# Performance work log

Hardware: AMD Instinct MI355X
Metric: run time of the kernel (lower is better)

## Reference

```python
import jax, jax.numpy as jnp
import numpy as np

K_GRAD = 20        # num_nbrs for gradient operator
K_NORMAL = 10      # knn for normal/basis estimation
GRAD_REG = 1e-3    # grad_reg (lambda)
KERNEL_WIDTH = 1.0 # grad_kernel_width
EPS = 1e-8
N1, N2 = 8192, 8192
CHANNELS = [3, 64, 128, 256]


def knn_idx(pos, k):
    # brute-force kNN incl. self (loop=True, target_to_source)
    sq = jnp.sum(pos * pos, axis=1)
    d2 = sq[:, None] + sq[None, :] - 2.0 * (pos @ pos.T)
    _, idx = jax.lax.top_k(-d2, k)
    return idx  # [N, k]


def estimate_basis(pos, nbr, orientation):
    rel = pos[nbr] - pos[:, None, :]              # [N,k,3]
    cov = jnp.einsum('nki,nkj->nij', rel, rel)    # [N,3,3] local PCA
    _, vecs = jnp.linalg.eigh(cov)                # ascending eigenvalues
    normal, x_basis = vecs[:, :, 0], vecs[:, :, 2]
    sign = jnp.where(jnp.sum(normal * orientation, -1, keepdims=True) < 0.0, -1.0, 1.0)
    normal = normal * sign                        # orient along `orientation`
    y_basis = jnp.cross(normal, x_basis)
    return normal, x_basis, y_basis


def build_grad_div(pos, x_basis, y_basis, nbr):
    # regularized, Gaussian-weighted least-squares fit of a linear function per neighborhood
    rel = pos[nbr] - pos[:, None, :]              # [N,k,3]
    u = jnp.einsum('nkd,nd->nk', rel, x_basis)    # tangent coords
    v = jnp.einsum('nkd,nd->nk', rel, y_basis)
    dist = jnp.sqrt(jnp.sum(rel * rel, -1) + EPS)
    h = jnp.mean(dist, axis=1, keepdims=True)     # per-point bandwidth
    w = jnp.exp(-(dist * dist) / ((KERNEL_WIDTH * h) ** 2 + EPS))
    B = jnp.stack([jnp.ones_like(u), u, v], -1)   # [N,k,3] design matrix
    BtW = jnp.swapaxes(B, 1, 2) * w[:, None, :]   # [N,3,k]
    A = BtW @ B + GRAD_REG * jnp.eye(3, dtype=pos.dtype)
    C = jnp.linalg.solve(A, BtW)                  # [N,3,k] LS coefficients
    Gx, Gy = C[:, 1, :], C[:, 2, :]               # gradient stencils
    basis = jnp.stack([x_basis, y_basis], -1)     # [N,3,2]
    R = jnp.einsum('nda,nkdb->nkab', basis, basis[nbr])  # transport j->i, [N,k,2,2]
    return Gx, Gy, R


def grad_apply(Gx, Gy, nbr, f):
    fn = f[nbr]                                   # [N,k,C]
    return jnp.stack([jnp.einsum('nk,nkc->nc', Gx, fn),
                      jnp.einsum('nk,nkc->nc', Gy, fn)], 1)  # [N,2,C]


def div_apply(Gx, Gy, R, nbr, v):
    vt = jnp.einsum('nkab,nkbc->nkac', R, v[nbr])  # transported neighbor vectors
    return (jnp.einsum('nk,nkc->nc', Gx, vt[:, :, 0]) +
            jnp.einsum('nk,nkc->nc', Gy, vt[:, :, 1]))


def delta_conv(x, v, nbr, Gx, Gy, R, Ws, bs, Wv, bv, centralized):
    xn = x[nbr]
    if centralized:
        xn = xn - x[:, None, :]
    xmax = jnp.max(xn, axis=1)                    # max aggregation
    dv = div_apply(Gx, Gy, R, nbr, v)             # divergence
    Jv = jnp.stack([-v[:, 1], v[:, 0]], 1)        # 90-degree rotation
    cv = div_apply(Gx, Gy, R, nbr, Jv)            # curl = div(J v)
    x_out = jax.nn.relu(jnp.concatenate([xmax, dv, cv], -1) @ Ws + bs)
    if Wv is None:
        return x_out, v                            # last layer: scalar only
    gv = grad_apply(Gx, Gy, nbr, x_out)           # [N,2,Cout]
    vo = jnp.concatenate([v, gv], -1) @ Wv        # channel mix, no bias (equivariant)
    n = jnp.sqrt(jnp.sum(vo * vo, axis=1, keepdims=True) + EPS)
    vo = vo * (jax.nn.relu(n + bv) / (n + EPS))   # norm-gated vector nonlinearity
    return x_out, vo


def _forward(points, als_ppoints, params):
    pos = jnp.concatenate([points, als_ppoints], axis=0)  # [N,3]
    nbr = knn_idx(pos, K_GRAD)
    nbr_n = knn_idx(pos, K_NORMAL)
    _, xb, yb = estimate_basis(pos, nbr_n, orientation=pos)
    Gx, Gy, R = build_grad_div(pos, xb, yb, nbr)
    x = pos
    v = grad_apply(Gx, Gy, nbr, x)                # v = grad @ x
    out = []
    for i, (Ws, bs, Wv, bv) in enumerate(params):
        x, v = delta_conv(x, v, nbr, Gx, Gy, R, Ws, bs, Wv, bv, centralized=(i == 0))
        out.append(x)
    return tuple(out)


def setup_inputs():
    key = jax.random.key(0)
    ks = jax.random.split(key, 8)
    inp = {
        'points': jax.random.normal(ks[0], (N1, 3), jnp.float32),
        'als_ppoints': jax.random.normal(ks[1], (N2, 3), jnp.float32),
    }
    ki = 2
    for i in range(3):
        cin, cout = CHANNELS[i], CHANNELS[i + 1]
        inp[f'Ws{i}'] = jax.random.normal(ks[ki], (3 * cin, cout), jnp.float32) / np.sqrt(3.0 * cin)
        inp[f'bs{i}'] = jnp.zeros((cout,), jnp.float32)
        ki += 1
        if i < 2:
            inp[f'Wv{i}'] = jax.random.normal(ks[ki], (cin + cout, cout), jnp.float32) / np.sqrt(float(cin + cout))
            inp[f'bv{i}'] = jnp.zeros((cout,), jnp.float32)
            ki += 1
    return inp


def reference(points, als_ppoints, Ws0, bs0, Wv0, bv0, Ws1, bs1, Wv1, bv1, Ws2, bs2):
    params = [(Ws0, bs0, Wv0, bv0), (Ws1, bs1, Wv1, bv1), (Ws2, bs2, None, None)]
    return _forward(points, als_ppoints, params)
```

## Files before the change

### kernel.cpp

```cpp
#include <hip/hip_runtime.h>
#include <math.h>

#define NPTS 16384
#define KG 20
#define KN 10
#define KC 6
#define EPSF 1e-8f

#define GDIM 32
#define GL 4.75f
#define CW 0.296875f
#define GINV 3.3684210526f
#define RMAX 6

typedef __attribute__((ext_vector_type(8))) short short8v;
typedef __attribute__((ext_vector_type(4))) float floatx4;

__device__ __forceinline__ unsigned short f2bf(float v) {
  union { float f; unsigned u; } x;
  x.f = v;
  unsigned r = x.u + 0x7FFFu + ((x.u >> 16) & 1u);
  return (unsigned short)(r >> 16);
}

__device__ __forceinline__ float bf2f(unsigned short u) {
  union { unsigned u32; float f; } x;
  x.u32 = (unsigned)u << 16;
  return x.f;
}

#define KNN_INSERT(d2v, iv)                                                 \
  if ((d2v) < dist[KG - 1]) {                                               \
    dist[KG - 1] = (d2v); idx[KG - 1] = (iv);                               \
    _Pragma("unroll")                                                       \
    for (int s_ = KG - 1; s_ > 0; --s_) {                                   \
      if (dist[s_] < dist[s_ - 1]) {                                        \
        float td_ = dist[s_]; dist[s_] = dist[s_ - 1]; dist[s_ - 1] = td_;  \
        int ti_ = idx[s_]; idx[s_] = idx[s_ - 1]; idx[s_ - 1] = ti_;        \
      }                                                                     \
    }                                                                       \
  }

#define KNN_INSERTC(d2v, iv)                                                \
  if ((d2v) < dist[KC - 1]) {                                               \
    dist[KC - 1] = (d2v); idx[KC - 1] = (iv);                               \
    _Pragma("unroll")                                                       \
    for (int s_ = KC - 1; s_ > 0; --s_) {                                   \
      if (dist[s_] < dist[s_ - 1]) {                                        \
        float td_ = dist[s_]; dist[s_] = dist[s_ - 1]; dist[s_ - 1] = td_;  \
        int ti_ = idx[s_]; idx[s_] = idx[s_ - 1]; idx[s_ - 1] = ti_;        \
      }                                                                     \
    }                                                                       \
  }

__global__ __launch_bounds__(256) void posbin_kernel(const float* __restrict__ pts,
                                                     const float* __restrict__ als,
                                                     float4* __restrict__ pos4,
                                                     int* __restrict__ cell_count,
                                                     int* __restrict__ pt_cell) {
  int n = blockIdx.x * 256 + threadIdx.x;
  if (n >= NPTS) return;
  const float* src = (n < 8192) ? (pts + (size_t)n * 3) : (als + (size_t)(n - 8192) * 3);
  float x = src[0], y = src[1], z = src[2];
  pos4[n] = make_float4(x, y, z, 0.f);
  int cxi = (int)floorf((x + GL) * GINV); cxi = min(max(cxi, 0), GDIM - 1);
  int cyi = (int)floorf((y + GL) * GINV); cyi = min(max(cyi, 0), GDIM - 1);
  int czi = (int)floorf((z + GL) * GINV); czi = min(max(czi, 0), GDIM - 1);
  int c = (czi * GDIM + cyi) * GDIM + cxi;
  pt_cell[n] = c;
  atomicAdd(&cell_count[c], 1);
}

__global__ __launch_bounds__(256) void zero_kernel(int* __restrict__ cell_count,
                                                   int* __restrict__ fb_count) {
  int i = blockIdx.x * 256 + threadIdx.x;
  if (i < GDIM * GDIM * GDIM) cell_count[i] = 0;
  if (i == 0) *fb_count = 0;
}

__device__ __forceinline__ int cell_of(float x) {
  int c = (int)floorf((x + GL) * GINV);
  return min(max(c, 0), GDIM - 1);
}

__global__ __launch_bounds__(1024) void scan_kernel(const int* __restrict__ cell_count,
                                                    int* __restrict__ cell_start,
                                                    int* __restrict__ cell_cursor) {
  __shared__ int s[1024];
  int tid = threadIdx.x;
  int base = tid * 32;
  int local[32];
  int sum = 0;
#pragma unroll
  for (int i = 0; i < 32; ++i) { local[i] = cell_count[base + i]; sum += local[i]; }
  s[tid] = sum;
  __syncthreads();
  for (int off = 1; off < 1024; off <<= 1) {
    int v = (tid >= off) ? s[tid - off] : 0;
    __syncthreads();
    s[tid] += v;
    __syncthreads();
  }
  int run = s[tid] - sum;
#pragma unroll
  for (int i = 0; i < 32; ++i) {
    cell_start[base + i] = run;
    cell_cursor[base + i] = run;
    run += local[i];
  }
}

__global__ __launch_bounds__(256) void scatter_kernel(const float4* __restrict__ pos4,
                                                      const int* __restrict__ pt_cell,
                                                      int* __restrict__ cell_cursor,
                                                      float4* __restrict__ sorted4,
                                                      int* __restrict__ sortmap) {
  int i = blockIdx.x * 256 + threadIdx.x;
  if (i >= NPTS) return;
  int c = pt_cell[i];
  int dst = atomicAdd(&cell_cursor[c], 1);
  float4 p = pos4[i];
  p.w = __int_as_float(i);
  sorted4[dst] = p;
  sortmap[dst] = i;
}

__global__ __launch_bounds__(256) void knn_grid_kernel(const float4* __restrict__ sorted4,
                                                       const int* __restrict__ cell_start,
                                                       const int* __restrict__ cell_count,
                                                       int* __restrict__ nbr,
                                                       int* __restrict__ fb_list,
                                                       int* __restrict__ fb_count) {
  int lane = threadIdx.x & 63;
  int sub = lane >> 5;
  int sl = lane & 31;
  int qs = blockIdx.x * 8 + (threadIdx.x >> 6) * 2 + sub;
  if (qs >= NPTS) return;
  float4 p = sorted4[qs];
  int cx = cell_of(p.x), cy = cell_of(p.y), cz = cell_of(p.z);
  float dist[KC];
  int idx[KC];
#pragma unroll
  for (int i = 0; i < KC; ++i) { dist[i] = 3.4e38f; idx[i] = 0; }

  {
    int tot = 0;
    int x0 = max(cx - 1, 0), x1 = min(cx + 1, GDIM - 1);
    int zlo = max(cz - 1, 0), zhi = min(cz + 1, GDIM - 1);
    int ylo = max(cy - 1, 0), yhi = min(cy + 1, GDIM - 1);
    for (int z = zlo; z <= zhi; ++z) {
      for (int y = ylo; y <= yhi; ++y) {
        int c0 = (z * GDIM + y) * GDIM + x0;
        int c1 = (z * GDIM + y) * GDIM + x1;
        int beg = cell_start[c0];
        int end = cell_start[c1] + cell_count[c1];
        int off = (sl - tot) & 31;
        for (int j = beg + off; j < end; j += 32) {
          float4 sp = sorted4[j];
          float dx = sp.x - p.x, dy = sp.y - p.y, dz = sp.z - p.z;
          float d2 = dx * dx + dy * dy + dz * dz;
          KNN_INSERTC(d2, j);
        }
        tot += end - beg;
      }
    }
  }
  int done;
  {
    float b2 = CW * CW;
    int cnt = 0;
#pragma unroll
    for (int i = 0; i < KC; ++i) cnt += (dist[i] <= b2) ? 1 : 0;
#pragma unroll
    for (int s = 1; s < 32; s <<= 1) cnt += __shfl_xor(cnt, s, 64);
    done = (cnt >= KG) ? 1 : 0;
  }

  for (int r = 2; r <= RMAX && !done; ++r) {
    int side = 2 * r + 1;
    int nt = side * side;
    float rcp = 1.0f / (float)side;
    for (int t = sl; t < nt; t += 32) {
      int qz = (int)(((float)t + 0.5f) * rcp);
      int dz = qz - r;
      int dy = t - qz * side - r;
      int z = cz + dz, y = cy + dy;
      if (z < 0 || z >= GDIM || y < 0 || y >= GDIM) continue;
      int rowbase = (z * GDIM + y) * GDIM;
      if (dz == -r || dz == r || dy == -r || dy == r) {
        int xa = max(cx - r, 0), xb = min(cx + r, GDIM - 1);
        int beg = cell_start[rowbase + xa];
        int end = cell_start[rowbase + xb] + cell_count[rowbase + xb];
        for (int j = beg; j < end; ++j) {
          float4 sp = sorted4[j];
          float ddx = sp.x - p.x, ddy = sp.y - p.y, ddz = sp.z - p.z;
          float d2 = ddx * ddx + ddy * ddy + ddz * ddz;
          KNN_INSERTC(d2, j);
        }
      } else {
        int x = cx - r;
        if (x >= 0) {
          int c = rowbase + x;
          int beg = cell_start[c], end = beg + cell_count[c];
          for (int j = beg; j < end; ++j) {
            float4 sp = sorted4[j];
            float ddx = sp.x - p.x, ddy = sp.y - p.y, ddz = sp.z - p.z;
            float d2 = ddx * ddx + ddy * ddy + ddz * ddz;
            KNN_INSERTC(d2, j);
          }
        }
        x = cx + r;
        if (x < GDIM) {
          int c = rowbase + x;
          int beg = cell_start[c], end = beg + cell_count[c];
          for (int j = beg; j < end; ++j) {
            float4 sp = sorted4[j];
            float ddx = sp.x - p.x, ddy = sp.y - p.y, ddz = sp.z - p.z;
            float d2 = ddx * ddx + ddy * ddy + ddz * ddz;
            KNN_INSERTC(d2, j);
          }
        }
      }
    }
    float b = CW * (float)r;
    float b2 = b * b;
    int cnt = 0;
#pragma unroll
    for (int i = 0; i < KC; ++i) cnt += (dist[i] <= b2) ? 1 : 0;
#pragma unroll
    for (int s = 1; s < 32; s <<= 1) cnt += __shfl_xor(cnt, s, 64);
    if (cnt >= KG) done = 1;
  }

  int popc = 0, ovf = 0;
  for (int round = 0; round < KG; ++round) {
    unsigned long long key = ((unsigned long long)__float_as_uint(dist[0]) << 14) |
                             (unsigned long long)(unsigned)idx[0];
    unsigned long long m = key;
#pragma unroll
    for (int s = 1; s < 32; s <<= 1) {
      unsigned long long o = __shfl_xor(m, s, 64);
      if (o < m) m = o;
    }
    if (key == m) {
      nbr[(size_t)qs * KG + round] = (int)(m & 0x3FFF);
#pragma unroll
      for (int s = 0; s < KC - 1; ++s) { dist[s] = dist[s + 1]; idx[s] = idx[s + 1]; }
      dist[KC - 1] = 3.4e38f;
      idx[KC - 1] = 0;
      if (++popc == KC) ovf = 1;
    }
  }
#pragma unroll
  for (int s = 1; s < 32; s <<= 1) ovf |= __shfl_xor(ovf, s, 64);
  if ((ovf || !done) && sl == 0) {
    int s = atomicAdd(fb_count, 1);
    fb_list[s] = qs;
  }
}

__global__ __launch_bounds__(256) void knn_fb_kernel(const float4* __restrict__ sorted4,
                                                     const int* __restrict__ fb_list,
                                                     const int* __restrict__ fb_count,
                                                     int* __restrict__ nbr) {
  __shared__ unsigned long long lists[256 * KG];
  __shared__ unsigned long long heads[256];
  __shared__ unsigned long long winner;
  int tid = threadIdx.x;
  int cnt = *fb_count;
  for (int qi = blockIdx.x; qi < cnt; qi += gridDim.x) {
    int t = fb_list[qi];
    float4 p = sorted4[t];
    float dist[KG];
    int idx[KG];
#pragma unroll
    for (int i = 0; i < KG; ++i) { dist[i] = 3.4e38f; idx[i] = 0; }
    int j0 = tid * 64;
    for (int j = j0; j < j0 + 64; ++j) {
      float4 c = sorted4[j];
      float dx = c.x - p.x, dy = c.y - p.y, dz = c.z - p.z;
      float d2 = dx * dx + dy * dy + dz * dz;
      KNN_INSERT(d2, j);
    }
#pragma unroll
    for (int i = 0; i < KG; ++i)
      lists[tid * KG + i] = ((unsigned long long)__float_as_uint(dist[i]) << 22) |
                            ((unsigned long long)(unsigned)idx[i] << 8) |
                            (unsigned long long)tid;
    int hp = 0;
    __syncthreads();
    for (int round = 0; round < KG; ++round) {
      heads[tid] = (hp < KG) ? lists[tid * KG + hp] : ~0ull;
      __syncthreads();
      if (tid < 64) {
        unsigned long long m = heads[tid];
        unsigned long long o = heads[tid + 64];  if (o < m) m = o;
        o = heads[tid + 128]; if (o < m) m = o;
        o = heads[tid + 192]; if (o < m) m = o;
#pragma unroll
        for (int s = 32; s > 0; s >>= 1) {
          unsigned long long x = __shfl_xor(m, s, 64);
          if (x < m) m = x;
        }
        if (tid == 0) winner = m;
      }
      __syncthreads();
      unsigned long long w = winner;
      if (tid == (int)(w & 0xFF)) hp++;
      if (tid == 0) nbr[(size_t)t * KG + round] = (int)((w >> 8) & 0x3FFF);
      __syncthreads();
    }
  }
}

__global__ __launch_bounds__(256) void basis_kernel(const float4* __restrict__ sorted4,
                                                    const int* __restrict__ nbr,
                                                    float4* __restrict__ xb4,
                                                    float4* __restrict__ yb4) {
  int n = blockIdx.x * 256 + threadIdx.x;
  if (n >= NPTS) return;
  float4 p = sorted4[n];
  float c00 = 0, c01 = 0, c02 = 0, c11 = 0, c12 = 0, c22 = 0;
  for (int k = 0; k < KN; ++k) {
    int m = nbr[(size_t)n * KG + k];
    float4 pm = sorted4[m];
    float dx = pm.x - p.x, dy = pm.y - p.y, dz = pm.z - p.z;
    c00 += dx * dx; c01 += dx * dy; c02 += dx * dz;
    c11 += dy * dy; c12 += dy * dz; c22 += dz * dz;
  }
  float nx = 0.f, ny = 0.f, nz = 1.f;
  float p1 = c01 * c01 + c02 * c02 + c12 * c12;
  float qm = (c00 + c11 + c22) * (1.f / 3.f);
  float g0 = c00 - qm, g1 = c11 - qm, g2 = c22 - qm;
  float p2 = g0 * g0 + g1 * g1 + g2 * g2 + 2.f * p1;
  if (p2 > 1e-16f) {
    float pp = sqrtf(p2 * (1.f / 6.f));
    float inv = 1.f / pp;
    float b00 = g0 * inv, b11 = g1 * inv, b22 = g2 * inv;
    float b01 = c01 * inv, b02 = c02 * inv, b12 = c12 * inv;
    float detB = b00 * (b11 * b22 - b12 * b12) - b01 * (b01 * b22 - b12 * b02) +
                 b02 * (b01 * b12 - b11 * b02);
    float r = 0.5f * detB;
    r = fminf(1.f, fmaxf(-1.f, r));
    float phi = acosf(r) * (1.f / 3.f);
    float e1 = qm + 2.f * pp * __cosf(phi);
    float e3 = qm + 2.f * pp * __cosf(phi + 2.0943951023931953f);
    float e2 = 3.f * qm - e1 - e3;
    float a00 = c00 - e1, a11 = c11 - e1, a22 = c22 - e1;
    float f00 = c00 - e2, f11 = c11 - e2, f22 = c22 - e2;
    float u0 = a00 * f00 + c01 * c01 + c02 * c02;
    float u1 = c01 * f00 + a11 * c01 + c12 * c02;
    float u2 = c02 * f00 + c12 * c01 + a22 * c02;
    float v0 = a00 * c01 + c01 * f11 + c02 * c12;
    float v1 = c01 * c01 + a11 * f11 + c12 * c12;
    float v2 = c02 * c01 + c12 * f11 + a22 * c12;
    float w0 = a00 * c02 + c01 * c12 + c02 * f22;
    float w1 = c01 * c02 + a11 * c12 + c12 * f22;
    float w2 = c02 * c02 + c12 * c12 + a22 * f22;
    float nu = u0 * u0 + u1 * u1 + u2 * u2;
    float nv = v0 * v0 + v1 * v1 + v2 * v2;
    float nw = w0 * w0 + w1 * w1 + w2 * w2;
    float bx = u0, by = u1, bz = u2, bn = nu;
    if (nv > bn) { bx = v0; by = v1; bz = v2; bn = nv; }
    if (nw > bn) { bx = w0; by = w1; bz = w2; bn = nw; }
    if (bn > 1e-30f) {
      float s = 1.f / sqrtf(bn);
      nx = bx * s; ny = by * s; nz = bz * s;
    }
  }
  float dotp = nx * p.x + ny * p.y + nz * p.z;
  if (dotp < 0.f) { nx = -nx; ny = -ny; nz = -nz; }
  float ax = fabsf(nx), ay = fabsf(ny), az = fabsf(nz);
  float ex = 0.f, ey = 0.f, ez = 0.f;
  if (ax <= ay && ax <= az) ex = 1.f;
  else if (ay <= az) ey = 1.f;
  else ez = 1.f;
  float tx = ny * ez - nz * ey, ty = nz * ex - nx * ez, tz = nx * ey - ny * ex;
  float tn = 1.f / sqrtf(tx * tx + ty * ty + tz * tz);
  tx *= tn; ty *= tn; tz *= tn;
  float ux = ny * tz - nz * ty, uy = nz * tx - nx * tz, uz = nx * ty - ny * tx;
  xb4[n] = make_float4(tx, ty, tz, 0.f);
  yb4[n] = make_float4(ux, uy, uz, 0.f);
}

__global__ __launch_bounds__(256) void graddiv_kernel(const float4* __restrict__ sorted4,
                                                      const int* __restrict__ nbr,
                                                      const float4* __restrict__ xb4,
                                                      const float4* __restrict__ yb4,
                                                      float* __restrict__ Gx,
                                                      float* __restrict__ Gy,
                                                      float2* __restrict__ C2,
                                                      float* __restrict__ v0) {
  int n = blockIdx.x * 256 + threadIdx.x;
  if (n >= NPTS) return;
  float4 p = sorted4[n], xb = xb4[n], yb = yb4[n];
  float u[KG], vv[KG], w[KG];
  int mm[KG];
  float hsum = 0.f;
#pragma unroll
  for (int k = 0; k < KG; ++k) {
    int m = nbr[(size_t)n * KG + k];
    mm[k] = m;
    float4 pm = sorted4[m];
    float rx = pm.x - p.x, ry = pm.y - p.y, rz = pm.z - p.z;
    u[k] = rx * xb.x + ry * xb.y + rz * xb.z;
    vv[k] = rx * yb.x + ry * yb.y + rz * yb.z;
    float dd = sqrtf(rx * rx + ry * ry + rz * rz + EPSF);
    w[k] = dd; hsum += dd;
  }
  float h = hsum * (1.f / KG);
  float invden = 1.f / (h * h + EPSF);
  float A00 = 0, A01 = 0, A02 = 0, A11 = 0, A12 = 0, A22 = 0;
#pragma unroll
  for (int k = 0; k < KG; ++k) {
    float wk = __expf(-(w[k] * w[k]) * invden);
    w[k] = wk;
    A00 += wk; A01 += wk * u[k]; A02 += wk * vv[k];
    A11 += wk * u[k] * u[k]; A12 += wk * u[k] * vv[k];
    A22 += wk * vv[k] * vv[k];
  }
  A00 += 0.001f; A11 += 0.001f; A22 += 0.001f;
  float det = A00 * (A11 * A22 - A12 * A12) - A01 * (A01 * A22 - A12 * A02) +
              A02 * (A01 * A12 - A11 * A02);
  float idet = 1.f / det;
  float i10 = (A02 * A12 - A01 * A22) * idet;
  float i11 = (A00 * A22 - A02 * A02) * idet;
  float i12 = (A01 * A02 - A00 * A12) * idet;
  float i20 = (A01 * A12 - A02 * A11) * idet;
  float i21 = i12;
  float i22 = (A00 * A11 - A01 * A01) * idet;
  float a0x = 0, a0y = 0, a0z = 0, a1x = 0, a1y = 0, a1z = 0;
#pragma unroll
  for (int k = 0; k < KG; ++k) {
    float gx = w[k] * (i10 + i11 * u[k] + i12 * vv[k]);
    float gy = w[k] * (i20 + i21 * u[k] + i22 * vv[k]);
    Gx[(size_t)n * KG + k] = gx;
    Gy[(size_t)n * KG + k] = gy;
    int m = mm[k];
    float4 pm = sorted4[m];
    a0x += gx * pm.x; a0y += gx * pm.y; a0z += gx * pm.z;
    a1x += gy * pm.x; a1y += gy * pm.y; a1z += gy * pm.z;
    float4 xm = xb4[m], ym = yb4[m];
    float g3x = gx * xb.x + gy * yb.x;
    float g3y = gx * xb.y + gy * yb.y;
    float g3z = gx * xb.z + gy * yb.z;
    float ca = g3x * xm.x + g3y * xm.y + g3z * xm.z;
    float cb = g3x * ym.x + g3y * ym.y + g3z * ym.z;
    C2[(size_t)n * KG + k] = make_float2(ca, cb);
  }
  v0[((size_t)n * 2 + 0) * 3 + 0] = a0x;
  v0[((size_t)n * 2 + 0) * 3 + 1] = a0y;
  v0[((size_t)n * 2 + 0) * 3 + 2] = a0z;
  v0[((size_t)n * 2 + 1) * 3 + 0] = a1x;
  v0[((size_t)n * 2 + 1) * 3 + 1] = a1y;
  v0[((size_t)n * 2 + 1) * 3 + 2] = a1z;
}

template <int CENTRAL>
__global__ __launch_bounds__(256) void feat16_kernel(const float* __restrict__ x, int ldx,
                                                     int cin,
                                                     const float* __restrict__ v,
                                                     const int* __restrict__ nbr,
                                                     const float2* __restrict__ C2,
                                                     unsigned short* __restrict__ feat, int Kp) {
  int per = Kp - 2 * cin;
  int gid = blockIdx.x * 256 + threadIdx.x;
  if (gid >= NPTS * per) return;
  int n = gid / per;
  int c = gid - n * per;
  size_t fb = (size_t)n * Kp;
  if (c >= cin) {
    feat[fb + 3 * cin + (c - cin)] = 0;
    return;
  }
  float xc = x[(size_t)n * ldx + c];
  float xmax = -3.4e38f, dv = 0.f, cv = 0.f;
  for (int k = 0; k < KG; ++k) {
    int m = nbr[(size_t)n * KG + k];
    float2 cc = C2[(size_t)n * KG + k];
    float xm = x[(size_t)m * ldx + c];
    xmax = fmaxf(xmax, CENTRAL ? (xm - xc) : xm);
    float va = v[((size_t)m * 2 + 0) * cin + c];
    float vb = v[((size_t)m * 2 + 1) * cin + c];
    dv += cc.x * va + cc.y * vb;
    cv += cc.y * va - cc.x * vb;
  }
  feat[fb + c] = f2bf(xmax);
  feat[fb + cin + c] = f2bf(dv);
  feat[fb + 2 * cin + c] = f2bf(cv);
}

__global__ __launch_bounds__(256) void feat16v8_kernel(const unsigned short* __restrict__ x,
                                                       int cin,
                                                       const unsigned short* __restrict__ v,
                                                       const int* __restrict__ nbr,
                                                       const float2* __restrict__ C2,
                                                       unsigned short* __restrict__ feat) {
  int per = cin >> 3;
  int gid = blockIdx.x * 256 + threadIdx.x;
  if (gid >= NPTS * per) return;
  int n = gid / per;
  int c8 = (gid - n * per) << 3;
  float xmax[8], dv[8], cv[8];
#pragma unroll
  for (int i = 0; i < 8; ++i) { xmax[i] = -3.4e38f; dv[i] = 0.f; cv[i] = 0.f; }
  const int* nrow = nbr + (size_t)n * KG;
  const float2* crow = C2 + (size_t)n * KG;
#pragma unroll 4
  for (int k = 0; k < KG; ++k) {
    int m = nrow[k];
    float2 cc = crow[k];
    short8v xm = *reinterpret_cast<const short8v*>(x + (size_t)m * cin + c8);
    short8v va = *reinterpret_cast<const short8v*>(v + ((size_t)m * 2 + 0) * cin + c8);
    short8v vb = *reinterpret_cast<const short8v*>(v + ((size_t)m * 2 + 1) * cin + c8);
#pragma unroll
    for (int i = 0; i < 8; ++i) {
      float xf = bf2f((unsigned short)xm[i]);
      float af = bf2f((unsigned short)va[i]);
      float bf = bf2f((unsigned short)vb[i]);
      xmax[i] = fmaxf(xmax[i], xf);
      dv[i] += cc.x * af + cc.y * bf;
      cv[i] += cc.y * af - cc.x * bf;
    }
  }
  size_t fb = (size_t)n * (3 * cin);
  short8v o0, o1, o2;
#pragma unroll
  for (int i = 0; i < 8; ++i) {
    o0[i] = (short)f2bf(xmax[i]);
    o1[i] = (short)f2bf(dv[i]);
    o2[i] = (short)f2bf(cv[i]);
  }
  *reinterpret_cast<short8v*>(&feat[fb + c8]) = o0;
  *reinterpret_cast<short8v*>(&feat[fb + cin + c8]) = o1;
  *reinterpret_cast<short8v*>(&feat[fb + 2 * cin + c8]) = o2;
}

__global__ __launch_bounds__(256) void vin16_kernel(const float* __restrict__ v, int cin,
                                                    const unsigned short* __restrict__ xout,
                                                    int cout,
                                                    const int* __restrict__ nbr,
                                                    const float* __restrict__ Gx,
                                                    const float* __restrict__ Gy,
                                                    unsigned short* __restrict__ vinb, int Kp,
                                                    int total) {
  int gid = blockIdx.x * 256 + threadIdx.x;
  if (gid >= total) return;
  int n = gid / Kp;
  int c = gid - n * Kp;
  int K = cin + cout;
  unsigned short o0, o1;
  if (c < cin) {
    o0 = f2bf(v[((size_t)n * 2 + 0) * cin + c]);
    o1 = f2bf(v[((size_t)n * 2 + 1) * cin + c]);
  } else if (c < K) {
    int cc = c - cin;
    float a0 = 0.f, a1 = 0.f;
    for (int k = 0; k < KG; ++k) {
      int m = nbr[(size_t)n * KG + k];
      float f = bf2f(xout[(size_t)m * cout + cc]);
      a0 += Gx[(size_t)n * KG + k] * f;
      a1 += Gy[(size_t)n * KG + k] * f;
    }
    o0 = f2bf(a0);
    o1 = f2bf(a1);
  } else {
    o0 = 0; o1 = 0;
  }
  vinb[((size_t)n * 2 + 0) * Kp + c] = o0;
  vinb[((size_t)n * 2 + 1) * Kp + c] = o1;
}

__global__ __launch_bounds__(256) void vin16v8_kernel(const unsigned short* __restrict__ v,
                                                      int cin,
                                                      const unsigned short* __restrict__ xout,
                                                      int cout,
                                                      const int* __restrict__ nbr,
                                                      const float* __restrict__ Gx,
                                                      const float* __restrict__ Gy,
                                                      unsigned short* __restrict__ vinb,
                                                      int Kp) {
  int per = Kp >> 3;
  int gid = blockIdx.x * 256 + threadIdx.x;
  if (gid >= NPTS * per) return;
  int n = gid / per;
  int c8 = (gid - n * per) << 3;
  short8v o0, o1;
  if (c8 < cin) {
    o0 = *reinterpret_cast<const short8v*>(v + ((size_t)n * 2 + 0) * cin + c8);
    o1 = *reinterpret_cast<const short8v*>(v + ((size_t)n * 2 + 1) * cin + c8);
  } else {
    int cc8 = c8 - cin;
    float a0[8], a1[8];
#pragma unroll
    for (int i = 0; i < 8; ++i) { a0[i] = 0.f; a1[i] = 0.f; }
    const int* nrow = nbr + (size_t)n * KG;
    const float* gxr = Gx + (size_t)n * KG;
    const float* gyr = Gy + (size_t)n * KG;
#pragma unroll 4
    for (int k = 0; k < KG; ++k) {
      int m = nrow[k];
      float gx = gxr[k], gy = gyr[k];
      short8v f = *reinterpret_cast<const short8v*>(xout + (size_t)m * cout + cc8);
#pragma unroll
      for (int i = 0; i < 8; ++i) {
        float ff = bf2f((unsigned short)f[i]);
        a0[i] += gx * ff;
        a1[i] += gy * ff;
      }
    }
#pragma unroll
    for (int i = 0; i < 8; ++i) {
      o0[i] = (short)f2bf(a0[i]);
      o1[i] = (short)f2bf(a1[i]);
    }
  }
  *reinterpret_cast<short8v*>(&vinb[((size_t)n * 2 + 0) * Kp + c8]) = o0;
  *reinterpret_cast<short8v*>(&vinb[((size_t)n * 2 + 1) * Kp + c8]) = o1;
}

__device__ __forceinline__ void wprep_one(const float* W, unsigned short* Wt, int K, int Kp,
                                          int N, int i) {
  int n = i / Kp, k = i - n * Kp;
  Wt[i] = (k < K) ? f2bf(W[(size_t)k * N + n]) : (unsigned short)0;
}

__global__ __launch_bounds__(256) void wprep_all_kernel(const float* __restrict__ Ws0,
                                                        const float* __restrict__ Wv0,
                                                        const float* __restrict__ Ws1,
                                                        const float* __restrict__ Wv1,
                                                        const float* __restrict__ Ws2,
                                                        unsigned short* __restrict__ Wt_s0,
                                                        unsigned short* __restrict__ Wt_v0,
                                                        unsigned short* __restrict__ Wt_s1,
                                                        unsigned short* __restrict__ Wt_v1,
                                                        unsigned short* __restrict__ Wt_s2) {
  int gid = blockIdx.x * 256 + threadIdx.x;
  if (gid < 2048) wprep_one(Ws0, Wt_s0, 9, 32, 64, gid);
  else if (gid < 8192) wprep_one(Wv0, Wt_v0, 67, 96, 64, gid - 2048);
  else if (gid < 32768) wprep_one(Ws1, Wt_s1, 192, 192, 128, gid - 8192);
  else if (gid < 57344) wprep_one(Wv1, Wt_v1, 192, 192, 128, gid - 32768);
  else if (gid < 155648) wprep_one(Ws2, Wt_s2, 384, 384, 256, gid - 57344);
}

template <int MODE>
__global__ __launch_bounds__(256) void gemm16_kernel(const unsigned short* __restrict__ A,
                                                     const unsigned short* __restrict__ Bt,
                                                     const float* __restrict__ bias,
                                                     float* __restrict__ Cf,
                                                     unsigned short* __restrict__ Cb,
                                                     const int* __restrict__ rowmap,
                                                     int Kp, int Ncol) {
  int lane = threadIdx.x & 63;
  int wave = threadIdx.x >> 6;
  int rowBase = blockIdx.y * 64 + wave * 16;
  int colBase = blockIdx.x * 64;
  int lr = lane & 15;
  int kg = (lane >> 4) * 8;
  floatx4 acc0 = {0.f, 0.f, 0.f, 0.f};
  floatx4 acc1 = acc0, acc2 = acc0, acc3 = acc0;
  const unsigned short* arow = A + (size_t)(rowBase + lr) * Kp + kg;
  const unsigned short* b0p = Bt + (size_t)(colBase + lr) * Kp + kg;
  for (int k0 = 0; k0 < Kp; k0 += 32) {
    short8v a = *reinterpret_cast<const short8v*>(arow + k0);
    short8v b0 = *reinterpret_cast<const short8v*>(b0p + k0);
    short8v b1 = *reinterpret_cast<const short8v*>(b0p + (size_t)16 * Kp + k0);
    short8v b2 = *reinterpret_cast<const short8v*>(b0p + (size_t)32 * Kp + k0);
    short8v b3 = *reinterpret_cast<const short8v*>(b0p + (size_t)48 * Kp + k0);
    acc0 = __builtin_amdgcn_mfma_f32_16x16x32_bf16(a, b0, acc0, 0, 0, 0);
    acc1 = __builtin_amdgcn_mfma_f32_16x16x32_bf16(a, b1, acc1, 0, 0, 0);
    acc2 = __builtin_amdgcn_mfma_f32_16x16x32_bf16(a, b2, acc2, 0, 0, 0);
    acc3 = __builtin_amdgcn_mfma_f32_16x16x32_bf16(a, b3, acc3, 0, 0, 0);
  }
  int rsub = (lane >> 4) * 4;
  floatx4 accs[4] = {acc0, acc1, acc2, acc3};
  int orow[4];
  if (MODE == 0) {
#pragma unroll
    for (int r = 0; r < 4; ++r) orow[r] = rowmap[rowBase + rsub + r];
  }
#pragma unroll
  for (int nb = 0; nb < 4; ++nb) {
    int col = colBase + nb * 16 + lr;
    float bb = bias[col];
    if (MODE == 0) {
#pragma unroll
      for (int r = 0; r < 4; ++r) {
        int row = rowBase + rsub + r;
        float val = fmaxf(accs[nb][r] + bb, 0.f);
        Cf[(size_t)orow[r] * Ncol + col] = val;
        if (Cb) Cb[(size_t)row * Ncol + col] = f2bf(val);
      }
    } else {
#pragma unroll
      for (int pr = 0; pr < 2; ++pr) {
        float a0 = accs[nb][2 * pr], a1 = accs[nb][2 * pr + 1];
        float nrm = sqrtf(a0 * a0 + a1 * a1 + EPSF);
        float s = fmaxf(nrm + bb, 0.f) / (nrm + EPSF);
        int row = rowBase + rsub + 2 * pr;
        Cb[(size_t)row * Ncol + col] = f2bf(a0 * s);
        Cb[(size_t)(row + 1) * Ncol + col] = f2bf(a1 * s);
      }
    }
  }
}

extern "C" void kernel_launch(void* const* d_in, const int* in_sizes, int n_in,
                              void* d_out, int out_size, void* d_ws, size_t ws_size,
                              hipStream_t stream) {
  const float* pts = (const float*)d_in[0];
  const float* als = (const float*)d_in[1];
  const float* Ws0 = (const float*)d_in[2];
  const float* bs0 = (const float*)d_in[3];
  const float* Wv0 = (const float*)d_in[4];
  const float* bv0 = (const float*)d_in[5];
  const float* Ws1 = (const float*)d_in[6];
  const float* bs1 = (const float*)d_in[7];
  const float* Wv1 = (const float*)d_in[8];
  const float* bv1 = (const float*)d_in[9];
  const float* Ws2 = (const float*)d_in[10];
  const float* bs2 = (const float*)d_in[11];

  char* ws = (char*)d_ws;
  float4* pos4 = (float4*)(ws + 0);
  int* nbr = (int*)(ws + 262144);
  float4* xb4 = (float4*)(ws + 1572864);
  float4* yb4 = (float4*)(ws + 1835008);
  float* Gx = (float*)(ws + 2097152);
  float* Gy = (float*)(ws + 3407872);
  float2* C2 = (float2*)(ws + 4718592);
  float* v0f = (float*)(ws + 7340032);
  unsigned short* vb_a = (unsigned short*)(ws + 8388608);
  unsigned short* vb_b = (unsigned short*)(ws + 17825792);
  unsigned short* xb0m = (unsigned short*)(ws + 23068672);
  unsigned short* xb1m = (unsigned short*)(ws + 26214400);
  unsigned short* stg = (unsigned short*)(ws + 31457280);
  char* wtb = ws + 45088768;
  unsigned short* Wt_s0 = (unsigned short*)(wtb + 0);
  unsigned short* Wt_v0 = (unsigned short*)(wtb + 4096);
  unsigned short* Wt_s1 = (unsigned short*)(wtb + 16384);
  unsigned short* Wt_v1 = (unsigned short*)(wtb + 65536);
  unsigned short* Wt_s2 = (unsigned short*)(wtb + 114688);

  char* gws = ws + 46137344;
  int* cell_count = (int*)(gws + 0);
  int* cell_start = (int*)(gws + 131072);
  int* cell_cursor = (int*)(gws + 262144);
  int* pt_cell = (int*)(gws + 393216);
  int* fb_list = (int*)(gws + 458752);
  int* fb_count = (int*)(gws + 524288);
  float4* sorted4 = (float4*)(gws + 528384);
  int* sortmap = (int*)(gws + 790528);

  float* out0 = (float*)d_out;
  float* out1 = out0 + (size_t)NPTS * 64;
  float* out2 = out1 + (size_t)NPTS * 128;

  zero_kernel<<<(GDIM * GDIM * GDIM + 255) / 256, 256, 0, stream>>>(cell_count, fb_count);
  posbin_kernel<<<64, 256, 0, stream>>>(pts, als, pos4, cell_count, pt_cell);
  scan_kernel<<<1, 1024, 0, stream>>>(cell_count, cell_start, cell_cursor);
  scatter_kernel<<<64, 256, 0, stream>>>(pos4, pt_cell, cell_cursor, sorted4, sortmap);
  knn_grid_kernel<<<NPTS / 8, 256, 0, stream>>>(sorted4, cell_start, cell_count, nbr, fb_list,
                                                fb_count);
  knn_fb_kernel<<<128, 256, 0, stream>>>(sorted4, fb_list, fb_count, nbr);

  basis_kernel<<<64, 256, 0, stream>>>(sorted4, nbr, xb4, yb4);
  graddiv_kernel<<<64, 256, 0, stream>>>(sorted4, nbr, xb4, yb4, Gx, Gy, C2, v0f);

  wprep_all_kernel<<<608, 256, 0, stream>>>(Ws0, Wv0, Ws1, Wv1, Ws2, Wt_s0, Wt_v0, Wt_s1,
                                            Wt_v1, Wt_s2);

  feat16_kernel<1><<<(NPTS * 26 + 255) / 256, 256, 0, stream>>>((const float*)sorted4, 4, 3,
                                                                v0f, nbr, C2, stg, 32);
  gemm16_kernel<0><<<dim3(1, 256), 256, 0, stream>>>(stg, Wt_s0, bs0, out0, xb0m, sortmap, 32,
                                                     64);
  vin16_kernel<<<(NPTS * 96 + 255) / 256, 256, 0, stream>>>(v0f, 3, xb0m, 64, nbr, Gx, Gy, stg,
                                                            96, NPTS * 96);
  gemm16_kernel<1><<<dim3(1, 512), 256, 0, stream>>>(stg, Wt_v0, bv0, nullptr, vb_b, nullptr,
                                                     96, 64);

  feat16v8_kernel<<<NPTS * 8 / 256, 256, 0, stream>>>(xb0m, 64, vb_b, nbr, C2, stg);
  gemm16_kernel<0><<<dim3(2, 256), 256, 0, stream>>>(stg, Wt_s1, bs1, out1, xb1m, sortmap, 192,
                                                     128);
  vin16v8_kernel<<<NPTS * 24 / 256, 256, 0, stream>>>(vb_b, 64, xb1m, 128, nbr, Gx, Gy, stg,
                                                      192);
  gemm16_kernel<1><<<dim3(2, 512), 256, 0, stream>>>(stg, Wt_v1, bv1, nullptr, vb_a, nullptr,
                                                     192, 128);

  feat16v8_kernel<<<NPTS * 16 / 256, 256, 0, stream>>>(xb1m, 128, vb_a, nbr, C2, stg);
  gemm16_kernel<0><<<dim3(4, 256), 256, 0, stream>>>(stg, Wt_s2, bs2, out2, nullptr, sortmap,
                                                     384, 256);
}
```

Baseline: 290.8 us.

## Reorder kNN queries by cell occupancy to balance wavefront work

Adds a histogram and counting-sort pass that orders grid kNN queries by how many points share their cell, so queries with similar search cost land in the same wavefront and divergence drops. The zero kernel is replaced by a memset over cell_count and fb_count, which are placed next to each other. This adds two small kernels, one of them single-block, and makes the query reads indirect, which can reduce spatial locality between neighbouring queries.

```diff
diff --git a/kernel.cpp b/kernel.cpp
--- a/kernel.cpp
+++ b/kernel.cpp
@@ -53,6 +53,11 @@
     }                                                                       \
   }
 
+__device__ __forceinline__ int cell_of(float x) {
+  int c = (int)floorf((x + GL) * GINV);
+  return min(max(c, 0), GDIM - 1);
+}
+
 __global__ __launch_bounds__(256) void posbin_kernel(const float* __restrict__ pts,
                                                      const float* __restrict__ als,
                                                      float4* __restrict__ pos4,
@@ -63,24 +68,9 @@
   const float* src = (n < 8192) ? (pts + (size_t)n * 3) : (als + (size_t)(n - 8192) * 3);
   float x = src[0], y = src[1], z = src[2];
   pos4[n] = make_float4(x, y, z, 0.f);
-  int cxi = (int)floorf((x + GL) * GINV); cxi = min(max(cxi, 0), GDIM - 1);
-  int cyi = (int)floorf((y + GL) * GINV); cyi = min(max(cyi, 0), GDIM - 1);
-  int czi = (int)floorf((z + GL) * GINV); czi = min(max(czi, 0), GDIM - 1);
-  int c = (czi * GDIM + cyi) * GDIM + cxi;
+  int c = (cell_of(z) * GDIM + cell_of(y)) * GDIM + cell_of(x);
   pt_cell[n] = c;
   atomicAdd(&cell_count[c], 1);
-}
-
-__global__ __launch_bounds__(256) void zero_kernel(int* __restrict__ cell_count,
-                                                   int* __restrict__ fb_count) {
-  int i = blockIdx.x * 256 + threadIdx.x;
-  if (i < GDIM * GDIM * GDIM) cell_count[i] = 0;
-  if (i == 0) *fb_count = 0;
-}
-
-__device__ __forceinline__ int cell_of(float x) {
-  int c = (int)floorf((x + GL) * GINV);
-  return min(max(c, 0), GDIM - 1);
 }
 
 __global__ __launch_bounds__(1024) void scan_kernel(const int* __restrict__ cell_count,
@@ -125,17 +115,52 @@
   sortmap[dst] = i;
 }
 
+__global__ __launch_bounds__(256) void qhist_kernel(const float4* __restrict__ sorted4,
+                                                    const int* __restrict__ cell_count,
+                                                    int* __restrict__ bcur) {
+  __shared__ int hist[64];
+  int tid = threadIdx.x;
+  if (tid < 64) hist[tid] = 0;
+  __syncthreads();
+  for (int s = tid; s < NPTS; s += 256) {
+    float4 p = sorted4[s];
+    int c = (cell_of(p.z) * GDIM + cell_of(p.y)) * GDIM + cell_of(p.x);
+    int occ = min(cell_count[c], 63);
+    atomicAdd(&hist[occ], 1);
+  }
+  __syncthreads();
+  if (tid == 0) {
+    int run = 0;
+    for (int b = 0; b < 64; ++b) { bcur[b] = run; run += hist[b]; }
+  }
+}
+
+__global__ __launch_bounds__(256) void qorder_kernel(const float4* __restrict__ sorted4,
+                                                     const int* __restrict__ cell_count,
+                                                     int* __restrict__ bcur,
+                                                     int* __restrict__ qorder) {
+  int s = blockIdx.x * 256 + threadIdx.x;
+  if (s >= NPTS) return;
+  float4 p = sorted4[s];
+  int c = (cell_of(p.z) * GDIM + cell_of(p.y)) * GDIM + cell_of(p.x);
+  int occ = min(cell_count[c], 63);
+  int dst = atomicAdd(&bcur[occ], 1);
+  qorder[dst] = s;
+}
+
 __global__ __launch_bounds__(256) void knn_grid_kernel(const float4* __restrict__ sorted4,
                                                        const int* __restrict__ cell_start,
                                                        const int* __restrict__ cell_count,
+                                                       const int* __restrict__ qorder,
                                                        int* __restrict__ nbr,
                                                        int* __restrict__ fb_list,
                                                        int* __restrict__ fb_count) {
   int lane = threadIdx.x & 63;
   int sub = lane >> 5;
   int sl = lane & 31;
-  int qs = blockIdx.x * 8 + (threadIdx.x >> 6) * 2 + sub;
-  if (qs >= NPTS) return;
+  int qlin = blockIdx.x * 8 + (threadIdx.x >> 6) * 2 + sub;
+  if (qlin >= NPTS) return;
+  int qs = qorder[qlin];
   float4 p = sorted4[qs];
   int cx = cell_of(p.x), cy = cell_of(p.y), cz = cell_of(p.z);
   float dist[KC];
@@ -744,24 +769,28 @@
 
   char* gws = ws + 46137344;
   int* cell_count = (int*)(gws + 0);
-  int* cell_start = (int*)(gws + 131072);
-  int* cell_cursor = (int*)(gws + 262144);
-  int* pt_cell = (int*)(gws + 393216);
-  int* fb_list = (int*)(gws + 458752);
-  int* fb_count = (int*)(gws + 524288);
-  float4* sorted4 = (float4*)(gws + 528384);
-  int* sortmap = (int*)(gws + 790528);
+  int* fb_count = (int*)(gws + 131072);
+  int* cell_start = (int*)(gws + 135168);
+  int* cell_cursor = (int*)(gws + 266240);
+  int* pt_cell = (int*)(gws + 397312);
+  int* fb_list = (int*)(gws + 462848);
+  int* bcur = (int*)(gws + 528384);
+  float4* sorted4 = (float4*)(gws + 532480);
+  int* sortmap = (int*)(gws + 794624);
+  int* qorder = (int*)(gws + 860160);
 
   float* out0 = (float*)d_out;
   float* out1 = out0 + (size_t)NPTS * 64;
   float* out2 = out1 + (size_t)NPTS * 128;
 
-  zero_kernel<<<(GDIM * GDIM * GDIM + 255) / 256, 256, 0, stream>>>(cell_count, fb_count);
+  hipMemsetAsync(cell_count, 0, 131072 + 4, stream);
   posbin_kernel<<<64, 256, 0, stream>>>(pts, als, pos4, cell_count, pt_cell);
   scan_kernel<<<1, 1024, 0, stream>>>(cell_count, cell_start, cell_cursor);
   scatter_kernel<<<64, 256, 0, stream>>>(pos4, pt_cell, cell_cursor, sorted4, sortmap);
-  knn_grid_kernel<<<NPTS / 8, 256, 0, stream>>>(sorted4, cell_start, cell_count, nbr, fb_list,
-                                                fb_count);
+  qhist_kernel<<<1, 256, 0, stream>>>(sorted4, cell_count, bcur);
+  qorder_kernel<<<64, 256, 0, stream>>>(sorted4, cell_count, bcur, qorder);
+  knn_grid_kernel<<<NPTS / 8, 256, 0, stream>>>(sorted4, cell_start, cell_count, qorder, nbr,
+                                                fb_list, fb_count);
   knn_fb_kernel<<<128, 256, 0, stream>>>(sorted4, fb_list, fb_count, nbr);
 
   basis_kernel<<<64, 256, 0, stream>>>(sorted4, nbr, xb4, yb4);
```

New measurement: 418.9 us. 44.1% more time.
